# Optimization experiments

Hardware: AMD Instinct MI355X
Metric: run time of the kernel (lower is better)

Reference implementation:

```python
import jax, jax.numpy as jnp
import numpy as np

B, S, D = 4, 2048, 1024


def setup_inputs() -> dict:
    key = jax.random.key(0)
    kx, kq, kk, kv, km = jax.random.split(key, 5)
    bound = 1.0 / np.sqrt(D)  # torch Linear default init range
    X = jax.random.normal(kx, (B, S, D), dtype=jnp.float32)
    Wq = jax.random.uniform(kq, (D, D), jnp.float32, -bound, bound)
    Wk = jax.random.uniform(kk, (D, D), jnp.float32, -bound, bound)
    Wv = jax.random.uniform(kv, (D, D), jnp.float32, -bound, bound)
    masks = jax.random.randint(km, (B, S), 0, 2, dtype=jnp.int32)
    return {"X": X, "masks": masks, "Wq": Wq, "Wk": Wk, "Wv": Wv}


def reference(X, masks, Wq, Wk, Wv):
    n = X.shape[1]
    # mask construction: True where masked (padding OR future position)
    lookahead = jnp.triu(jnp.ones((n, n), dtype=bool), k=1)          # [S,S]
    pad = ~(masks.astype(bool))[:, None, :]                           # [B,1,S] -> key-side padding
    m = (pad | lookahead[None]).astype(X.dtype)                       # [B,S,S]

    # Linear layers (torch: y = x @ W.T)
    Q = jnp.einsum('bsd,ed->bse', X, Wq)
    K = jnp.einsum('bsd,ed->bse', X, Wk)
    V = jnp.einsum('bsd,ed->bse', X, Wv)

    # cosine-normalized attention scores, multiplied (not added) by the mask
    Qn = Q / jnp.linalg.norm(Q, axis=-1, keepdims=True)
    Kn = K / jnp.linalg.norm(K, axis=-1, keepdims=True)
    scores = jnp.einsum('bqd,bkd->bqk', Qn, Kn) * m                   # [B,S,S]
    return jnp.einsum('bqk,bkd->bqd', scores, V)
```

## Files before the change

### kernel.cpp

```cpp
#include <hip/hip_runtime.h>
#include <hip/hip_bf16.h>

#define B_ 4
#define S_ 2048
#define D_ 1024
#define MTOT (B_ * S_)

typedef __attribute__((ext_vector_type(8))) short bf16x8;
typedef __attribute__((ext_vector_type(4))) float f32x4;

__device__ __forceinline__ unsigned short f2bf(float f) {
  union { float f; unsigned int u; } v; v.f = f;
  unsigned int r = v.u + 0x7FFFu + ((v.u >> 16) & 1u);
  return (unsigned short)(r >> 16);
}
__device__ __forceinline__ float bf2f(unsigned short u) {
  union { unsigned int u; float f; } v; v.u = ((unsigned int)u) << 16;
  return v.f;
}

__global__ void cvt_f32_bf16(const float* __restrict__ in, unsigned short* __restrict__ outp, int n4) {
  int i = blockIdx.x * blockDim.x + threadIdx.x;
  if (i >= n4) return;
  float4 v = ((const float4*)in)[i];
  ushort4 o;
  o.x = f2bf(v.x); o.y = f2bf(v.y); o.z = f2bf(v.z); o.w = f2bf(v.w);
  ((ushort4*)outp)[i] = o;
}

__global__ __launch_bounds__(256) void rownorm_bf16(const unsigned short* __restrict__ QKb,
                                                    unsigned short* __restrict__ Qn,
                                                    unsigned short* __restrict__ Kn) {
  int row = blockIdx.x;
  int half = blockIdx.y;
  int tid = threadIdx.x;
  ushort4 u = *(const ushort4*)(QKb + (long)row * 2048 + half * 1024 + tid * 4);
  float x0 = bf2f(u.x), x1 = bf2f(u.y), x2 = bf2f(u.z), x3 = bf2f(u.w);
  float ss = x0 * x0 + x1 * x1 + x2 * x2 + x3 * x3;
#pragma unroll
  for (int o = 1; o < 64; o <<= 1) ss += __shfl_xor(ss, o);
  __shared__ float wsum[4];
  if ((tid & 63) == 0) wsum[tid >> 6] = ss;
  __syncthreads();
  float rn = rsqrtf(wsum[0] + wsum[1] + wsum[2] + wsum[3]);
  ushort4 o;
  o.x = f2bf(x0 * rn); o.y = f2bf(x1 * rn); o.z = f2bf(x2 * rn); o.w = f2bf(x3 * rn);
  unsigned short* op = half ? Kn : Qn;
  *(ushort4*)(op + (long)row * D_ + tid * 4) = o;
}

#define BM 128
#define BN 128
#define BK 32

#define GLDS16(g, l)                                                                   \
  __builtin_amdgcn_global_load_lds((const __attribute__((address_space(1))) void*)(g), \
                                   (__attribute__((address_space(3))) void*)(l), 16, 0, 0)

template <int EPI>
__global__ __launch_bounds__(256, 2) void gemm_bt(const unsigned short* __restrict__ A,
                                                  const unsigned short* __restrict__ B,
                                                  void* __restrict__ Cv, int N, int K,
                                                  long strideA, long strideB, long strideC,
                                                  const int* __restrict__ masks) {
  __shared__ __align__(16) short lA[2][BM * BK];
  __shared__ __align__(16) short lB[2][BN * BK];
  int z = blockIdx.z;
  const unsigned short* Ab = A + (long)z * strideA;
  const unsigned short* Bb = B + (long)z * strideB;
  int tid = threadIdx.x;
  int lane = tid & 63, w = tid >> 6;
  int wr = w >> 1, wc = w & 1;
  int brow = blockIdx.x * BM, bcol = blockIdx.y * BN;

  f32x4 acc[4][4];
#pragma unroll
  for (int m = 0; m < 4; m++)
#pragma unroll
    for (int n = 0; n < 4; n++) acc[m][n] = (f32x4){0.f, 0.f, 0.f, 0.f};

  const unsigned short* ga = Ab + (long)(brow + (tid >> 2)) * K + ((tid & 3) << 3);
  const unsigned short* gb = Bb + (long)(bcol + (tid >> 2)) * K + ((tid & 3) << 3);
  int fr = lane & 15, fq = lane >> 4;

#define STAGE(buf)                                          \
  do {                                                      \
    char* la = (char*)(&lA[buf][0]) + ((tid >> 6) << 10);   \
    char* lb = (char*)(&lB[buf][0]) + ((tid >> 6) << 10);   \
    GLDS16(ga, la);                                         \
    GLDS16(ga + (long)64 * K, la + 4096);                   \
    GLDS16(gb, lb);                                         \
    GLDS16(gb + (long)64 * K, lb + 4096);                   \
    ga += BK;                                               \
    gb += BK;                                               \
  } while (0)

  STAGE(0);
  __syncthreads();

  int nt = K / BK;
  for (int t = 0; t < nt; ++t) {
    int cur = t & 1;
    if (t + 1 < nt) STAGE(cur ^ 1);
    const short* pa = &lA[cur][(wr * 64 + fr) * BK + fq * 8];
    const short* pb = &lB[cur][(wc * 64 + fr) * BK + fq * 8];
    bf16x8 af[4], bv[4];
#pragma unroll
    for (int m = 0; m < 4; m++) af[m] = *(const bf16x8*)(pa + m * 16 * BK);
#pragma unroll
    for (int n = 0; n < 4; n++) bv[n] = *(const bf16x8*)(pb + n * 16 * BK);
#pragma unroll
    for (int m = 0; m < 4; m++)
#pragma unroll
      for (int n = 0; n < 4; n++)
        acc[m][n] = __builtin_amdgcn_mfma_f32_16x16x32_bf16(af[m], bv[n], acc[m][n], 0, 0, 0);
    __syncthreads();
  }
#undef STAGE

  long cbase = (long)z * strideC;
#pragma unroll
  for (int m = 0; m < 4; m++) {
#pragma unroll
    for (int n = 0; n < 4; n++) {
#pragma unroll
      for (int r = 0; r < 4; r++) {
        int grow = brow + wr * 64 + m * 16 + fq * 4 + r;
        int gcol = bcol + wc * 64 + n * 16 + fr;
        float v = acc[m][n][r];
        if constexpr (EPI == 0) {
          ((float*)Cv)[cbase + (long)grow * N + gcol] = v;
        } else if constexpr (EPI == 1) {
          ((unsigned short*)Cv)[cbase + (long)grow * N + gcol] = f2bf(v);
        } else if constexpr (EPI == 2) {
          bool keep = (gcol > grow) || (masks[z * S_ + gcol] == 0);
          ((unsigned short*)Cv)[cbase + (long)grow * N + gcol] = keep ? f2bf(v) : (unsigned short)0;
        } else {
          int b = gcol >> 11, s = gcol & (S_ - 1);
          ((unsigned short*)Cv)[(long)b * D_ * S_ + (long)grow * S_ + s] = f2bf(v);
        }
      }
    }
  }
}

extern "C" void kernel_launch(void* const* d_in, const int* in_sizes, int n_in, void* d_out,
                              int out_size, void* d_ws, size_t ws_size, hipStream_t stream) {
  (void)in_sizes; (void)n_in; (void)out_size; (void)ws_size;
  const float* X = (const float*)d_in[0];
  const int* masks = (const int*)d_in[1];
  const float* Wq = (const float*)d_in[2];
  const float* Wk = (const float*)d_in[3];
  const float* Wv = (const float*)d_in[4];
  float* out = (float*)d_out;

  char* ws = (char*)d_ws;
  unsigned short* Xb = (unsigned short*)ws;   ws += (long)MTOT * D_ * 2;
  unsigned short* Wqkb = (unsigned short*)ws; ws += (long)2 * D_ * D_ * 2;
  unsigned short* Wvb = (unsigned short*)ws;  ws += (long)D_ * D_ * 2;
  unsigned short* QKb = (unsigned short*)ws;  ws += (long)MTOT * 2 * D_ * 2;
  unsigned short* Qn = (unsigned short*)ws;   ws += (long)MTOT * D_ * 2;
  unsigned short* Kn = (unsigned short*)ws;   ws += (long)MTOT * D_ * 2;
  unsigned short* Vt = (unsigned short*)ws;   ws += (long)MTOT * D_ * 2;
  unsigned short* Sm = (unsigned short*)ws;   ws += (long)B_ * S_ * S_ * 2;

  int n4x = MTOT * D_ / 4;
  cvt_f32_bf16<<<(n4x + 255) / 256, 256, 0, stream>>>(X, Xb, n4x);
  int n4w = D_ * D_ / 4;
  cvt_f32_bf16<<<(n4w + 255) / 256, 256, 0, stream>>>(Wq, Wqkb, n4w);
  cvt_f32_bf16<<<(n4w + 255) / 256, 256, 0, stream>>>(Wk, Wqkb + (long)D_ * D_, n4w);
  cvt_f32_bf16<<<(n4w + 255) / 256, 256, 0, stream>>>(Wv, Wvb, n4w);

  dim3 blk(256);
  gemm_bt<1><<<dim3(MTOT / BM, 2 * D_ / BN, 1), blk, 0, stream>>>(Xb, Wqkb, QKb, 2 * D_, D_,
                                                                  0, 0, 0, nullptr);
  rownorm_bf16<<<dim3(MTOT, 2), 256, 0, stream>>>(QKb, Qn, Kn);
  gemm_bt<3><<<dim3(D_ / BM, MTOT / BN, 1), blk, 0, stream>>>(Wvb, Xb, Vt, MTOT, D_,
                                                              0, 0, 0, nullptr);
  gemm_bt<2><<<dim3(S_ / BM, S_ / BN, B_), blk, 0, stream>>>(Qn, Kn, Sm, S_, D_,
                                                             (long)S_ * D_, (long)S_ * D_,
                                                             (long)S_ * S_, masks);
  gemm_bt<0><<<dim3(S_ / BM, D_ / BN, B_), blk, 0, stream>>>(Sm, Vt, out, D_, S_,
                                                             (long)S_ * S_, (long)D_ * S_,
                                                             (long)S_ * D_, nullptr);
}
```

Measured before the change: 201.2 us.

## Triple-buffer GEMM pipeline, fuse QKV projection, merge casts, narrow PV tile

Merges the four f32-to-bf16 conversion launches into one kernel. Fuses the QK and V projections into a single GEMM whose epilogue writes Q, K and transposed V into separate planes. Replaces the GEMM's double buffer with a three-slot LDS pipeline that waits on explicit vmcnt counts and raw barriers, and raises the occupancy hint to 3. Uses a 128x64 tile for the final score-times-V GEMM to get more blocks. These aim to cut launch overhead and memory-latency stalls, at the cost of more LDS per block and hand-tuned wait counts that must stay correct.

Result: slower. 229.4 us (+14.0%).

```diff
diff --git a/kernel.cpp b/kernel.cpp
--- a/kernel.cpp
+++ b/kernel.cpp
@@ -19,22 +19,39 @@
   return v.f;
 }
 
-__global__ void cvt_f32_bf16(const float* __restrict__ in, unsigned short* __restrict__ outp, int n4) {
-  int i = blockIdx.x * blockDim.x + threadIdx.x;
-  if (i >= n4) return;
-  float4 v = ((const float4*)in)[i];
+__global__ __launch_bounds__(256) void cvt_all(const float* __restrict__ X,
+                                               const float* __restrict__ Wq,
+                                               const float* __restrict__ Wk,
+                                               const float* __restrict__ Wv,
+                                               unsigned short* __restrict__ Xb,
+                                               unsigned short* __restrict__ Wqkv) {
+  long i = (long)blockIdx.x * 256 + threadIdx.x;
+  const float* src;
+  unsigned short* dst;
+  long off;
+  if (i < 2097152L) {
+    src = X; dst = Xb; off = i;
+  } else {
+    long j = i - 2097152L;
+    int w = (int)(j >> 18);
+    off = j & 262143L;
+    src = (w == 0) ? Wq : (w == 1) ? Wk : Wv;
+    dst = Wqkv + (long)w * 1048576L;
+  }
+  float4 v = ((const float4*)src)[off];
   ushort4 o;
   o.x = f2bf(v.x); o.y = f2bf(v.y); o.z = f2bf(v.z); o.w = f2bf(v.w);
-  ((ushort4*)outp)[i] = o;
-}
-
-__global__ __launch_bounds__(256) void rownorm_bf16(const unsigned short* __restrict__ QKb,
+  ((ushort4*)dst)[off] = o;
+}
+
+__global__ __launch_bounds__(256) void rownorm_bf16(const unsigned short* __restrict__ QKraw,
                                                     unsigned short* __restrict__ Qn,
                                                     unsigned short* __restrict__ Kn) {
   int row = blockIdx.x;
   int half = blockIdx.y;
   int tid = threadIdx.x;
-  ushort4 u = *(const ushort4*)(QKb + (long)row * 2048 + half * 1024 + tid * 4);
+  const unsigned short* src = QKraw + (long)half * MTOT * D_;
+  ushort4 u = *(const ushort4*)(src + (long)row * D_ + tid * 4);
   float x0 = bf2f(u.x), x1 = bf2f(u.y), x2 = bf2f(u.z), x3 = bf2f(u.w);
   float ss = x0 * x0 + x1 * x1 + x2 * x2 + x3 * x3;
 #pragma unroll
@@ -49,72 +66,89 @@
   *(ushort4*)(op + (long)row * D_ + tid * 4) = o;
 }
 
-#define BM 128
-#define BN 128
-#define BK 32
 
 #define GLDS16(g, l)                                                                   \
   __builtin_amdgcn_global_load_lds((const __attribute__((address_space(1))) void*)(g), \
                                    (__attribute__((address_space(3))) void*)(l), 16, 0, 0)
 
-template <int EPI>
-__global__ __launch_bounds__(256, 2) void gemm_bt(const unsigned short* __restrict__ A,
+template <int EPI, int BN>
+__global__ __launch_bounds__(256, 3) void gemm_tb(const unsigned short* __restrict__ A,
                                                   const unsigned short* __restrict__ B,
                                                   void* __restrict__ Cv, int N, int K,
                                                   long strideA, long strideB, long strideC,
                                                   const int* __restrict__ masks) {
-  __shared__ __align__(16) short lA[2][BM * BK];
-  __shared__ __align__(16) short lB[2][BN * BK];
-  int z = blockIdx.z;
+  constexpr int NB = BN / 32;
+  constexpr int LD = (BN == 128) ? 4 : 3;
+  constexpr int ASLOT = 128 * 32 * 2;
+  constexpr int BSLOT = BN * 32 * 2;
+  __shared__ __align__(16) short lA[3][128 * 32];
+  __shared__ __align__(16) short lB[3][BN * 32];
+
+  const int z = blockIdx.z;
   const unsigned short* Ab = A + (long)z * strideA;
   const unsigned short* Bb = B + (long)z * strideB;
-  int tid = threadIdx.x;
-  int lane = tid & 63, w = tid >> 6;
-  int wr = w >> 1, wc = w & 1;
-  int brow = blockIdx.x * BM, bcol = blockIdx.y * BN;
-
-  f32x4 acc[4][4];
+  const int t = threadIdx.x;
+  const int lane = t & 63, w = t >> 6;
+  const int wr = w >> 1, wc = w & 1;
+  const int fr = lane & 15, fq = lane >> 4;
+  const int brow = blockIdx.x * 128, bcol = blockIdx.y * BN;
+
+  const char* gAs = (const char*)(Ab + (long)(brow + (t >> 2)) * K) + ((t & 3) << 4);
+  const char* gBs = (const char*)(Bb + (long)(bcol + (t >> 2)) * K) + ((t & 3) << 4);
+  const long astr = (long)64 * K * 2;
+  char* lAw = (char*)&lA[0][0] + (w << 10);
+  char* lBw = (char*)&lB[0][0] + (w << 10);
+
+#define STAGE(slot)                                                 \
+  do {                                                              \
+    GLDS16(gAs, lAw + (slot) * ASLOT);                              \
+    GLDS16(gAs + astr, lAw + (slot) * ASLOT + 4096);                \
+    GLDS16(gBs, lBw + (slot) * BSLOT);                              \
+    if constexpr (BN == 128) GLDS16(gBs + astr, lBw + (slot) * BSLOT + 4096); \
+    gAs += 64;                                                      \
+    gBs += 64;                                                      \
+  } while (0)
+
+  f32x4 acc[4][NB];
 #pragma unroll
   for (int m = 0; m < 4; m++)
 #pragma unroll
-    for (int n = 0; n < 4; n++) acc[m][n] = (f32x4){0.f, 0.f, 0.f, 0.f};
-
-  const unsigned short* ga = Ab + (long)(brow + (tid >> 2)) * K + ((tid & 3) << 3);
-  const unsigned short* gb = Bb + (long)(bcol + (tid >> 2)) * K + ((tid & 3) << 3);
-  int fr = lane & 15, fq = lane >> 4;
-
-#define STAGE(buf)                                          \
-  do {                                                      \
-    char* la = (char*)(&lA[buf][0]) + ((tid >> 6) << 10);   \
-    char* lb = (char*)(&lB[buf][0]) + ((tid >> 6) << 10);   \
-    GLDS16(ga, la);                                         \
-    GLDS16(ga + (long)64 * K, la + 4096);                   \
-    GLDS16(gb, lb);                                         \
-    GLDS16(gb + (long)64 * K, lb + 4096);                   \
-    ga += BK;                                               \
-    gb += BK;                                               \
-  } while (0)
-
+    for (int n = 0; n < NB; n++) acc[m][n] = (f32x4){0.f, 0.f, 0.f, 0.f};
+
+  const int NT = K / 32;
   STAGE(0);
-  __syncthreads();
-
-  int nt = K / BK;
-  for (int t = 0; t < nt; ++t) {
-    int cur = t & 1;
-    if (t + 1 < nt) STAGE(cur ^ 1);
-    const short* pa = &lA[cur][(wr * 64 + fr) * BK + fq * 8];
-    const short* pb = &lB[cur][(wc * 64 + fr) * BK + fq * 8];
-    bf16x8 af[4], bv[4];
-#pragma unroll
-    for (int m = 0; m < 4; m++) af[m] = *(const bf16x8*)(pa + m * 16 * BK);
-#pragma unroll
-    for (int n = 0; n < 4; n++) bv[n] = *(const bf16x8*)(pb + n * 16 * BK);
+  STAGE(1);
+  asm volatile("s_waitcnt vmcnt(%0)" ::"i"(LD) : "memory");
+  __builtin_amdgcn_s_barrier();
+  __builtin_amdgcn_sched_barrier(0);
+
+  int cs = 0, ss = 2;
+  const int arow0 = (wr * 64 + fr) * 32 + fq * 8;
+  const int brow0 = (wc * (BN / 2) + fr) * 32 + fq * 8;
+  for (int kt = 0; kt < NT; ++kt) {
+    if (kt + 2 < NT) STAGE(ss);
+    const short* pa = (const short*)((const char*)&lA[0][0] + cs * ASLOT) + arow0;
+    const short* pb = (const short*)((const char*)&lB[0][0] + cs * BSLOT) + brow0;
+    bf16x8 af[4], bv[NB];
+#pragma unroll
+    for (int m = 0; m < 4; m++) af[m] = *(const bf16x8*)(pa + m * 16 * 32);
+#pragma unroll
+    for (int n = 0; n < NB; n++) bv[n] = *(const bf16x8*)(pb + n * 16 * 32);
 #pragma unroll
     for (int m = 0; m < 4; m++)
 #pragma unroll
-      for (int n = 0; n < 4; n++)
+      for (int n = 0; n < NB; n++)
         acc[m][n] = __builtin_amdgcn_mfma_f32_16x16x32_bf16(af[m], bv[n], acc[m][n], 0, 0, 0);
-    __syncthreads();
+    if (kt + 1 < NT) {
+      if (kt + 2 < NT)
+        asm volatile("s_waitcnt vmcnt(%0)" ::"i"(LD) : "memory");
+      else
+        asm volatile("s_waitcnt vmcnt(0)" ::: "memory");
+      __builtin_amdgcn_s_barrier();
+      __builtin_amdgcn_sched_barrier(0);
+    }
+    cs = (cs == 2) ? 0 : cs + 1;
+    ss = (ss == 2) ? 0 : ss + 1;
   }
 #undef STAGE
 
@@ -122,22 +156,28 @@
 #pragma unroll
   for (int m = 0; m < 4; m++) {
 #pragma unroll
-    for (int n = 0; n < 4; n++) {
+    for (int n = 0; n < NB; n++) {
 #pragma unroll
       for (int r = 0; r < 4; r++) {
         int grow = brow + wr * 64 + m * 16 + fq * 4 + r;
-        int gcol = bcol + wc * 64 + n * 16 + fr;
+        int gcol = bcol + wc * (BN / 2) + n * 16 + fr;
         float v = acc[m][n][r];
         if constexpr (EPI == 0) {
           ((float*)Cv)[cbase + (long)grow * N + gcol] = v;
         } else if constexpr (EPI == 1) {
-          ((unsigned short*)Cv)[cbase + (long)grow * N + gcol] = f2bf(v);
-        } else if constexpr (EPI == 2) {
+          unsigned short* base = (unsigned short*)Cv;
+          int seg = gcol >> 10, c = gcol & 1023;
+          if (seg == 0) {
+            base[(long)grow * D_ + c] = f2bf(v);
+          } else if (seg == 1) {
+            base[(long)MTOT * D_ + (long)grow * D_ + c] = f2bf(v);
+          } else {
+            int b = grow >> 11, s = grow & (S_ - 1);
+            base[(long)2 * MTOT * D_ + (long)b * D_ * S_ + (long)c * S_ + s] = f2bf(v);
+          }
+        } else {
           bool keep = (gcol > grow) || (masks[z * S_ + gcol] == 0);
           ((unsigned short*)Cv)[cbase + (long)grow * N + gcol] = keep ? f2bf(v) : (unsigned short)0;
-        } else {
-          int b = gcol >> 11, s = gcol & (S_ - 1);
-          ((unsigned short*)Cv)[(long)b * D_ * S_ + (long)grow * S_ + s] = f2bf(v);
         }
       }
     }
@@ -155,32 +195,21 @@
   float* out = (float*)d_out;
 
   char* ws = (char*)d_ws;
-  unsigned short* Xb = (unsigned short*)ws;   ws += (long)MTOT * D_ * 2;
-  unsigned short* Wqkb = (unsigned short*)ws; ws += (long)2 * D_ * D_ * 2;
-  unsigned short* Wvb = (unsigned short*)ws;  ws += (long)D_ * D_ * 2;
-  unsigned short* QKb = (unsigned short*)ws;  ws += (long)MTOT * 2 * D_ * 2;
-  unsigned short* Qn = (unsigned short*)ws;   ws += (long)MTOT * D_ * 2;
-  unsigned short* Kn = (unsigned short*)ws;   ws += (long)MTOT * D_ * 2;
-  unsigned short* Vt = (unsigned short*)ws;   ws += (long)MTOT * D_ * 2;
-  unsigned short* Sm = (unsigned short*)ws;   ws += (long)B_ * S_ * S_ * 2;
-
-  int n4x = MTOT * D_ / 4;
-  cvt_f32_bf16<<<(n4x + 255) / 256, 256, 0, stream>>>(X, Xb, n4x);
-  int n4w = D_ * D_ / 4;
-  cvt_f32_bf16<<<(n4w + 255) / 256, 256, 0, stream>>>(Wq, Wqkb, n4w);
-  cvt_f32_bf16<<<(n4w + 255) / 256, 256, 0, stream>>>(Wk, Wqkb + (long)D_ * D_, n4w);
-  cvt_f32_bf16<<<(n4w + 255) / 256, 256, 0, stream>>>(Wv, Wvb, n4w);
-
-  dim3 blk(256);
-  gemm_bt<1><<<dim3(MTOT / BM, 2 * D_ / BN, 1), blk, 0, stream>>>(Xb, Wqkb, QKb, 2 * D_, D_,
-                                                                  0, 0, 0, nullptr);
-  rownorm_bf16<<<dim3(MTOT, 2), 256, 0, stream>>>(QKb, Qn, Kn);
-  gemm_bt<3><<<dim3(D_ / BM, MTOT / BN, 1), blk, 0, stream>>>(Wvb, Xb, Vt, MTOT, D_,
-                                                              0, 0, 0, nullptr);
-  gemm_bt<2><<<dim3(S_ / BM, S_ / BN, B_), blk, 0, stream>>>(Qn, Kn, Sm, S_, D_,
-                                                             (long)S_ * D_, (long)S_ * D_,
-                                                             (long)S_ * S_, masks);
-  gemm_bt<0><<<dim3(S_ / BM, D_ / BN, B_), blk, 0, stream>>>(Sm, Vt, out, D_, S_,
-                                                             (long)S_ * S_, (long)D_ * S_,
-                                                             (long)S_ * D_, nullptr);
-}
+  unsigned short* Xb = (unsigned short*)ws;     ws += (long)MTOT * D_ * 2;
+  unsigned short* Wqkv = (unsigned short*)ws;   ws += (long)3 * D_ * D_ * 2;
+  unsigned short* QKVraw = (unsigned short*)ws; ws += (long)3 * MTOT * D_ * 2;
+  unsigned short* Qn = (unsigned short*)ws;     ws += (long)MTOT * D_ * 2;
+  unsigned short* Kn = (unsigned short*)ws;     ws += (long)MTOT * D_ * 2;
+  unsigned short* Sm = (unsigned short*)ws;     ws += (long)B_ * S_ * S_ * 2;
+  unsigned short* Vt = QKVraw + (long)2 * MTOT * D_;
+
+  cvt_all<<<11264, 256, 0, stream>>>(X, Wq, Wk, Wv, Xb, Wqkv);
+
+  gemm_tb<1, 128><<<dim3(MTOT / 128, 3 * D_ / 128, 1), 256, 0, stream>>>(
+      Xb, Wqkv, QKVraw, 3 * D_, D_, 0, 0, 0, nullptr);
+  rownorm_bf16<<<dim3(MTOT, 2), 256, 0, stream>>>(QKVraw, Qn, Kn);
+  gemm_tb<2, 128><<<dim3(S_ / 128, S_ / 128, B_), 256, 0, stream>>>(
+      Qn, Kn, Sm, S_, D_, (long)S_ * D_, (long)S_ * D_, (long)S_ * S_, masks);
+  gemm_tb<0, 64><<<dim3(S_ / 128, D_ / 64, B_), 256, 0, stream>>>(
+      Sm, Vt, out, D_, S_, (long)S_ * S_, (long)D_ * S_, (long)S_ * D_, nullptr);
+}
```
